# Performance work log

Measured on AMD Instinct MI355X. Metric: run time of the kernel, lower is better.

Reference implementation:

```python
import jax, jax.numpy as jnp
import numpy as np

D = 256  # feature_dim
NQ = 512
NK = 512


def setup_inputs() -> dict:
    key = jax.random.key(0)
    ks = jax.random.split(key, 12)
    s = 0.05
    return {
        "x": jax.random.normal(ks[0], (1, D, NQ), dtype=jnp.float32),
        "source": jax.random.normal(ks[1], (1, D, NK), dtype=jnp.float32),
        "dist": jax.random.normal(ks[2], (1, D, NQ * NK), dtype=jnp.float32),
        "mask": jax.random.randint(ks[3], (NQ, NK), 0, 2).astype(jnp.bool_),
        # MLPAttention mlp: channels [3D, D, 1] (1x1 convs == per-position matmuls)
        "aW1": jax.random.normal(ks[4], (D, 3 * D), dtype=jnp.float32) * s,
        "ab1": jax.random.normal(ks[5], (D,), dtype=jnp.float32) * s,
        "aW2": jax.random.normal(ks[6], (1, D), dtype=jnp.float32) * s,
        "ab2": jax.random.normal(ks[7], (1,), dtype=jnp.float32) * s,
        # merge mlp: channels [2D, 2D, D], last bias initialized to 0
        "mW1": jax.random.normal(ks[8], (2 * D, 2 * D), dtype=jnp.float32) * s,
        "mb1": jax.random.normal(ks[9], (2 * D,), dtype=jnp.float32) * s,
        "mW2": jax.random.normal(ks[10], (D, 2 * D), dtype=jnp.float32) * s,
        "mb2": jnp.zeros((D,), dtype=jnp.float32),
    }


def _conv1x1(W, b, x):
    # Conv1d(kernel_size=1): (out,in) @ (b,in,n) -> (b,out,n)
    return jnp.einsum('oc,bcn->bon', W, x) + b[None, :, None]


def reference(x, source, dist, mask, aW1, ab1, aW2, ab2, mW1, mb1, mW2, mb2):
    nq, nk = x.shape[-1], source.shape[-1]
    d = x.shape[1]
    # broadcast query over keys and key over queries, flatten to (1, d, nq*nk)
    qb = jnp.broadcast_to(x[:, :, :, None], (1, d, nq, nk)).reshape(1, d, nq * nk)
    kb = jnp.broadcast_to(source[:, :, None, :], (1, d, nq, nk)).reshape(1, d, nq * nk)
    feat = jnp.concatenate([qb, kb, dist], axis=1)  # (1, 3d, nq*nk)
    h = jax.nn.relu(_conv1x1(aW1, ab1, feat))       # (1, d, nq*nk)
    scores = _conv1x1(aW2, ab2, h).reshape(1, nq, nk)
    # boolean-mask branch: push masked-out entries far below the min
    neg = jax.lax.stop_gradient(scores.min()) - 20.0
    scores = scores + neg * (~mask).astype(scores.dtype)[None]
    prob = jax.nn.softmax(scores, axis=-1)
    message = jnp.einsum('bnm,bdm->bdn', prob, source)  # value == source
    # merge MLP on concat([x, message])
    cat = jnp.concatenate([x, message], axis=1)  # (1, 2d, nq)
    h2 = jax.nn.relu(_conv1x1(mW1, mb1, cat))
    out = _conv1x1(mW2, mb2, h2)  # (1, d, nq)
    return (out, scores)
```

## Files before the change

kernel.cpp:

```cpp
#include <hip/hip_runtime.h>
#include <stdint.h>

#define D_ 256
#define NQ_ 512
#define NK_ 512
#define NP_ (NQ_*NK_)

typedef __attribute__((ext_vector_type(8))) __bf16 bf16x8;
typedef __attribute__((ext_vector_type(4))) float f32x4;

__device__ __forceinline__ unsigned short f2bf(float f) {
  unsigned u = __builtin_bit_cast(unsigned, f);
  u += 0x7FFFu + ((u >> 16) & 1u);
  return (unsigned short)(u >> 16);
}
__device__ __forceinline__ unsigned encf(float f) {
  unsigned u = __builtin_bit_cast(unsigned, f);
  return (u & 0x80000000u) ? ~u : (u | 0x80000000u);
}
__device__ __forceinline__ float decf(unsigned e) {
  unsigned u = (e & 0x80000000u) ? (e ^ 0x80000000u) : ~e;
  return __builtin_bit_cast(float, u);
}

template<int EPI, int KTILES>
__device__ __forceinline__ void gemm_body(
    const unsigned short* __restrict__ A, int lda,
    const unsigned short* __restrict__ B, int ldb,
    const float* __restrict__ bias,
    void* __restrict__ Dst, int ldd, int nTilesN, int bid) {
  const int t = threadIdx.x, w = t >> 6, l = t & 63, l15 = l & 15, g = l >> 4;
  const int bm = bid / nTilesN, bn = bid % nTilesN;
  const int m0 = bm*64 + w*16, n0 = bn*64;
  const unsigned short* Ap = A + (size_t)(m0 + l15)*lda + g*8;
  const unsigned short* Bp = B + (size_t)(n0 + l15)*ldb + g*8;
  f32x4 acc[4];
  #pragma unroll
  for (int n = 0; n < 4; ++n) acc[n] = (f32x4){0.f,0.f,0.f,0.f};
  #pragma unroll 2
  for (int kk = 0; kk < KTILES; ++kk) {
    bf16x8 a = *(const bf16x8*)(Ap + kk*32);
    #pragma unroll
    for (int n = 0; n < 4; ++n) {
      bf16x8 b = *(const bf16x8*)(Bp + (size_t)n*16*ldb + kk*32);
      acc[n] = __builtin_amdgcn_mfma_f32_16x16x32_bf16(a, b, acc[n], 0, 0, 0);
    }
  }
  #pragma unroll
  for (int n = 0; n < 4; ++n) {
    const int col = n0 + n*16 + l15;
    const float bc = (EPI & 4) ? bias[col] : 0.f;
    #pragma unroll
    for (int r = 0; r < 4; ++r) {
      const int m = m0 + g*4 + r;
      float v = acc[n][r] + bc;
      if (EPI & 8) v += bias[m];
      if (EPI & 2) v = fmaxf(v, 0.f);
      if (EPI & 1) ((unsigned short*)Dst)[(size_t)m*ldd + col] = f2bf(v);
      else         ((float*)Dst)[(size_t)m*ldd + col] = v;
    }
  }
}

template<int EPI, int KTILES>
__global__ __launch_bounds__(256) void gemm_k(
    const unsigned short* __restrict__ A, int lda,
    const unsigned short* __restrict__ B, int ldb,
    const float* __restrict__ bias,
    void* __restrict__ Dst, int ldd, int nTilesN) {
  gemm_body<EPI, KTILES>(A, lda, B, ldb, bias, Dst, ldd, nTilesN, blockIdx.x);
}

__global__ __launch_bounds__(256) void kprep(
    const unsigned* __restrict__ maskw, unsigned* __restrict__ wsMin,
    unsigned* __restrict__ wsFlag,
    const float* __restrict__ aW1, const float* __restrict__ source,
    const float* __restrict__ x, const float* __restrict__ mW1,
    const float* __restrict__ mW2,
    unsigned short* __restrict__ Cb, unsigned short* __restrict__ srcbf,
    unsigned short* __restrict__ mW1b, unsigned short* __restrict__ mW2b,
    unsigned short* __restrict__ aW1A, unsigned short* __restrict__ aW1B,
    unsigned short* __restrict__ catT, unsigned short* __restrict__ srcT) {
  __shared__ float tile[64][65];
  const int b = blockIdx.x, t = threadIdx.x;
  if (b == 0) {
    if (t < 64) {
      unsigned a01 = 1, af = 1;
      for (int i = 0; i < 4; ++i) {
        unsigned v = maskw[t*4 + i];
        a01 &= (v == 0u || v == 1u) ? 1u : 0u;
        af  &= (v == 0u || v == 0x3f800000u) ? 1u : 0u;
      }
      unsigned long long b01 = __ballot(a01 != 0), bf = __ballot(af != 0);
      if (t == 0) {
        *wsFlag = (b01 == ~0ull) ? 1u : ((bf == ~0ull) ? 2u : 0u);
        *wsMin = 0xFFFFFFFFu;
      }
    }
    return;
  }
  if (b < 705) {
    const int bb = b - 1;
    const float* src; unsigned short* dst;
    if (bb < 64)        { int j = bb*1024 + t*4;       int e=j>>8, c=j&255; src = aW1 + e*768 + 512 + c; dst = Cb + j; }
    else if (bb < 192)  { int j = (bb-64)*1024 + t*4;  src = source + j;    dst = srcbf + j; }
    else if (bb < 448)  { int j = (bb-192)*1024 + t*4; src = mW1 + j;       dst = mW1b + j; }
    else if (bb < 576)  { int j = (bb-448)*1024 + t*4; src = mW2 + j;       dst = mW2b + j; }
    else if (bb < 640)  { int j = (bb-576)*1024 + t*4; int e=j>>8, c=j&255; src = aW1 + e*768 + c;       dst = aW1A + j; }
    else                { int j = (bb-640)*1024 + t*4; int e=j>>8, c=j&255; src = aW1 + e*768 + 256 + c; dst = aW1B + j; }
    const float4 v = *(const float4*)src;
    ushort4 o; o.x=f2bf(v.x); o.y=f2bf(v.y); o.z=f2bf(v.z); o.w=f2bf(v.w);
    *(ushort4*)dst = o;
    return;
  }
  const float* src; unsigned short* dst; int ldd, bid;
  if (b < 737) { src = x;      dst = catT; ldd = 512; bid = b - 705; }
  else         { src = source; dst = srcT; ldd = 256; bid = b - 737; }
  const int bd = bid >> 3, bq = bid & 7;
  const int r = t >> 4, c4 = (t & 15) * 4;
  #pragma unroll
  for (int rr = 0; rr < 4; ++rr) {
    int dl = rr*16 + r;
    float4 v = *(const float4*)(src + (size_t)(bd*64 + dl)*512 + bq*64 + c4);
    tile[dl][c4+0] = v.x; tile[dl][c4+1] = v.y; tile[dl][c4+2] = v.z; tile[dl][c4+3] = v.w;
  }
  __syncthreads();
  #pragma unroll
  for (int rr = 0; rr < 4; ++rr) {
    int j = rr*16 + r;
    ushort4 o;
    o.x = f2bf(tile[c4+0][j]); o.y = f2bf(tile[c4+1][j]);
    o.z = f2bf(tile[c4+2][j]); o.w = f2bf(tile[c4+3][j]);
    *(ushort4*)(dst + (size_t)(bq*64 + j)*ldd + bd*64 + c4) = o;
  }
}

__global__ __launch_bounds__(256) void kprep2(
    const unsigned short* __restrict__ catT, const unsigned short* __restrict__ aW1A,
    const float* __restrict__ ab1, float* __restrict__ Up,
    const unsigned short* __restrict__ aW1B, const unsigned short* __restrict__ srcT,
    float* __restrict__ Vm) {
  if (blockIdx.x < 32)
    gemm_body<4, 8>(catT, 512, aW1A, 256, ab1, (void*)Up, 256, 4, blockIdx.x);
  else
    gemm_body<0, 8>(aW1B, 256, srcT, 256, (const float*)nullptr, (void*)Vm, 512, 8, blockIdx.x - 32);
}

__device__ __forceinline__ void loads8(float (&s)[8], const float* __restrict__ dbase,
                                       int kk, int quad1, int quad2) {
  #pragma unroll
  for (int i = 0; i < 4; ++i) s[i]   = dbase[(size_t)(kk*32 + quad1*4 + i) * NP_];
  #pragma unroll
  for (int i = 0; i < 4; ++i) s[4+i] = dbase[(size_t)(kk*32 + quad2*4 + i) * NP_];
}
__device__ __forceinline__ void cvtwrite(unsigned char* __restrict__ buf, const float (&s)[8],
                                         int l, int quad1, int quad2) {
  const int key = (l >> 1) & 3;
  {
    unsigned lo = (unsigned)f2bf(s[0]) | ((unsigned)f2bf(s[1]) << 16);
    unsigned hi = (unsigned)f2bf(s[2]) | ((unsigned)f2bf(s[3]) << 16);
    *(uint2*)(buf + l*64 + ((((quad1>>1) ^ key) << 4) | ((quad1 & 1) << 3))) = make_uint2(lo, hi);
  }
  {
    unsigned lo = (unsigned)f2bf(s[4]) | ((unsigned)f2bf(s[5]) << 16);
    unsigned hi = (unsigned)f2bf(s[6]) | ((unsigned)f2bf(s[7]) << 16);
    *(uint2*)(buf + l*64 + ((((quad2>>1) ^ key) << 4) | ((quad2 & 1) << 3))) = make_uint2(lo, hi);
  }
}
__device__ __forceinline__ void computeStep(f32x4 (&acc)[4][4],
                                            const unsigned short* __restrict__ Abase,
                                            const unsigned char* __restrict__ buf,
                                            int kk, int l15, int g) {
  bf16x8 a[4], bfrag[4];
  #pragma unroll
  for (int m = 0; m < 4; ++m)
    a[m] = *(const bf16x8*)(Abase + (size_t)m*16*256 + kk*32);
  #pragma unroll
  for (int n = 0; n < 4; ++n) {
    const int p = n*16 + l15;
    bfrag[n] = *(const bf16x8*)(buf + p*64 + ((g ^ ((p >> 1) & 3)) << 4));
  }
  #pragma unroll
  for (int m = 0; m < 4; ++m)
    #pragma unroll
    for (int n = 0; n < 4; ++n)
      acc[m][n] = __builtin_amdgcn_mfma_f32_16x16x32_bf16(a[m], bfrag[n], acc[m][n], 0, 0, 0);
}

__global__ __launch_bounds__(256, 3) void kscores(
    const float* __restrict__ dist, const unsigned short* __restrict__ Cb,
    const float* __restrict__ Up, const float* __restrict__ Vm,
    const float* __restrict__ aW2, const float* __restrict__ ab2,
    float* __restrict__ outScores, unsigned* __restrict__ wsMin) {
  __shared__ __align__(16) unsigned char ldsB[2][64*64];
  __shared__ float u_s[256], aw2_s[256];
  __shared__ float red[4][64];

  const int t = threadIdx.x;
  const int w = t >> 6;
  const int l = t & 63;
  const int l15 = l & 15;
  const int g = l >> 4;

  const int bid = blockIdx.x;
  const int p0 = ((bid & 7) * 512 + (bid >> 3)) * 64;
  const int q  = p0 >> 9;
  const int k0 = p0 & 511;

  const int quad1 = (w + g) & 3;
  const int quad2 = quad1 + 4;

  const float* dbase = dist + (size_t)p0 + l;
  const unsigned short* Abase = Cb + (size_t)(w*64 + l15)*256 + g*8;

  float sA[8], sB[8];
  loads8(sA, dbase, 0, quad1, quad2);
  loads8(sB, dbase, 1, quad1, quad2);

  u_s[t]   = Up[q*256 + t];
  aw2_s[t] = aW2[t];

  f32x4 acc[4][4];
  #pragma unroll
  for (int m = 0; m < 4; ++m)
    #pragma unroll
    for (int n = 0; n < 4; ++n) acc[m][n] = (f32x4){0.f, 0.f, 0.f, 0.f};

  cvtwrite(ldsB[0], sA, l, quad1, quad2);
  __syncthreads();

  #pragma unroll
  for (int kk = 0; kk < 8; ++kk) {
    const int b = kk & 1;
    if (kk < 6) {
      if (b == 0) loads8(sA, dbase, kk + 2, quad1, quad2);
      else        loads8(sB, dbase, kk + 2, quad1, quad2);
    }
    computeStep(acc, Abase, ldsB[b], kk, l15, g);
    if (kk < 7) {
      if (b == 0) cvtwrite(ldsB[1], sB, l, quad1, quad2);
      else        cvtwrite(ldsB[0], sA, l, quad1, quad2);
    }
    __syncthreads();
  }

  float part[4];
  #pragma unroll
  for (int n = 0; n < 4; ++n) {
    int j = k0 + n*16 + l15;
    float s = 0.f;
    #pragma unroll
    for (int m = 0; m < 4; ++m) {
      #pragma unroll
      for (int r = 0; r < 4; ++r) {
        int e = w*64 + m*16 + g*4 + r;
        float gv = acc[m][n][r] + u_s[e] + Vm[e*512 + j];
        s += aw2_s[e] * fmaxf(gv, 0.f);
      }
    }
    s += __shfl_xor(s, 16);
    s += __shfl_xor(s, 32);
    part[n] = s;
  }
  if (l < 16) {
    #pragma unroll
    for (int n = 0; n < 4; ++n) red[w][n*16 + l] = part[n];
  }
  __syncthreads();
  if (t < 64) {
    float s = red[0][t] + red[1][t] + red[2][t] + red[3][t] + ab2[0];
    outScores[p0 + t] = s;
    float mn = s;
    #pragma unroll
    for (int off = 32; off; off >>= 1) mn = fminf(mn, __shfl_xor(mn, off));
    if (t == 0) atomicMin(wsMin, encf(mn));
  }
}

__global__ __launch_bounds__(256) void ksoftmax(
    const void* __restrict__ maskp,
    const unsigned* __restrict__ wsMin, const unsigned* __restrict__ wsFlag,
    float* __restrict__ scores, unsigned short* __restrict__ prob) {
  __shared__ float srow[512];
  __shared__ float redl[8];
  const int t = threadIdx.x, w = t >> 6, l = t & 63;
  const int q = blockIdx.x;
  const float neg = decf(*wsMin) - 20.0f;
  const unsigned flag = *wsFlag;

  for (int k = t; k < 512; k += 256) {
    float raw = scores[q*512 + k];
    bool mv;
    if (flag == 1)      mv = ((const int*)maskp)[q*512 + k] != 0;
    else if (flag == 2) mv = ((const float*)maskp)[q*512 + k] != 0.f;
    else                mv = ((const unsigned char*)maskp)[q*512 + k] != 0;
    float ms = raw + (mv ? 0.f : neg);
    scores[q*512 + k] = ms;
    srow[k] = ms;
  }
  __syncthreads();
  float lm = fmaxf(srow[t], srow[t + 256]);
  #pragma unroll
  for (int off = 32; off; off >>= 1) lm = fmaxf(lm, __shfl_xor(lm, off));
  if (l == 0) redl[w] = lm;
  __syncthreads();
  float rmax = fmaxf(fmaxf(redl[0], redl[1]), fmaxf(redl[2], redl[3]));
  float e0 = __expf(srow[t] - rmax), e1 = __expf(srow[t + 256] - rmax);
  float ls = e0 + e1;
  #pragma unroll
  for (int off = 32; off; off >>= 1) ls += __shfl_xor(ls, off);
  if (l == 0) redl[4 + w] = ls;
  __syncthreads();
  float inv = 1.0f / (redl[4] + redl[5] + redl[6] + redl[7]);
  prob[q*512 + t]       = f2bf(e0 * inv);
  prob[q*512 + t + 256] = f2bf(e1 * inv);
}

extern "C" void kernel_launch(void* const* d_in, const int* in_sizes, int n_in,
                              void* d_out, int out_size, void* d_ws, size_t ws_size,
                              hipStream_t stream) {
  const float* x      = (const float*)d_in[0];
  const float* source = (const float*)d_in[1];
  const float* dist   = (const float*)d_in[2];
  const void*  mask   = (const void*)d_in[3];
  const float* aW1    = (const float*)d_in[4];
  const float* ab1    = (const float*)d_in[5];
  const float* aW2    = (const float*)d_in[6];
  const float* ab2    = (const float*)d_in[7];
  const float* mW1    = (const float*)d_in[8];
  const float* mb1    = (const float*)d_in[9];
  const float* mW2    = (const float*)d_in[10];
  const float* mb2    = (const float*)d_in[11];

  float* outMain = (float*)d_out;
  float* scores  = outMain + 256*512;

  char* ws = (char*)d_ws;
  unsigned* wsMin  = (unsigned*)ws;
  unsigned* wsFlag = wsMin + 1;
  unsigned short* Cb    = (unsigned short*)(ws + 1024);
  float*          Up    = (float*)(ws + 132096);
  float*          Vm    = (float*)(ws + 656384);
  unsigned short* srcbf = (unsigned short*)(ws + 1180672);
  unsigned short* srcT  = (unsigned short*)(ws + 1442816);
  unsigned short* mW1b  = (unsigned short*)(ws + 1704960);
  unsigned short* mW2b  = (unsigned short*)(ws + 2229248);
  unsigned short* aW1A  = (unsigned short*)(ws + 2491392);
  unsigned short* aW1B  = (unsigned short*)(ws + 2622464);
  unsigned short* catT  = (unsigned short*)(ws + 2753536);
  unsigned short* prob  = (unsigned short*)(ws + 3277824);
  unsigned short* h2T   = (unsigned short*)(ws + 3802112);

  hipLaunchKernelGGL(kprep, dim3(769), dim3(256), 0, stream,
                     (const unsigned*)mask, wsMin, wsFlag, aW1, source, x, mW1, mW2,
                     Cb, srcbf, mW1b, mW2b, aW1A, aW1B, catT, srcT);
  hipLaunchKernelGGL(kprep2, dim3(64), dim3(256), 0, stream,
                     catT, aW1A, ab1, Up, aW1B, srcT, Vm);
  hipLaunchKernelGGL(kscores, dim3(4096), dim3(256), 0, stream,
                     dist, Cb, Up, Vm, aW2, ab2, scores, wsMin);
  hipLaunchKernelGGL(ksoftmax, dim3(512), dim3(256), 0, stream,
                     mask, wsMin, wsFlag, scores, prob);
  hipLaunchKernelGGL((gemm_k<1, 16>), dim3(32), dim3(256), 0, stream,
                     prob, 512, srcbf, 512, (const float*)nullptr, (void*)(catT + 256), 512, 4);
  hipLaunchKernelGGL((gemm_k<7, 16>), dim3(64), dim3(256), 0, stream,
                     catT, 512, mW1b, 512, mb1, (void*)h2T, 512, 8);
  hipLaunchKernelGGL((gemm_k<8, 16>), dim3(32), dim3(256), 0, stream,
                     mW2b, 512, h2T, 512, mb2, (void*)outMain, 512, 8);
}
```

Measured before the change: 186.5 us.

## Deepen dist prefetch to three stages and double-buffer A fragments

Restructures the kscores main loop to keep three register buffers of dist loads in flight instead of two, and prefetches the next step's A (weight) fragments into registers while the current step's MFMAs run. Explicit sched_barriers, an lgkmcnt wait and a raw s_barrier replace the trailing __syncthreads so the LDS write, next global loads and compute are ordered manually. This aims to hide global-load latency of the dist stream, at the cost of more VGPRs, which may reduce occupancy under launch_bounds(256,3). Because only one barrier now separates the LDS write of a buffer from later reads, reusing that buffer two steps later may be racy.

```diff
diff --git a/kernel.cpp b/kernel.cpp
--- a/kernel.cpp
+++ b/kernel.cpp
@@ -167,14 +167,16 @@
     *(uint2*)(buf + l*64 + ((((quad2>>1) ^ key) << 4) | ((quad2 & 1) << 3))) = make_uint2(lo, hi);
   }
 }
-__device__ __forceinline__ void computeStep(f32x4 (&acc)[4][4],
-                                            const unsigned short* __restrict__ Abase,
-                                            const unsigned char* __restrict__ buf,
-                                            int kk, int l15, int g) {
-  bf16x8 a[4], bfrag[4];
+__device__ __forceinline__ void loadA(bf16x8 (&a)[4], const unsigned short* __restrict__ Abase,
+                                      int kk) {
   #pragma unroll
   for (int m = 0; m < 4; ++m)
     a[m] = *(const bf16x8*)(Abase + (size_t)m*16*256 + kk*32);
+}
+__device__ __forceinline__ void computeStep(f32x4 (&acc)[4][4], const bf16x8 (&a)[4],
+                                            const unsigned char* __restrict__ buf,
+                                            int l15, int g) {
+  bf16x8 bfrag[4];
   #pragma unroll
   for (int n = 0; n < 4; ++n) {
     const int p = n*16 + l15;
@@ -213,54 +215,55 @@
   const float* dbase = dist + (size_t)p0 + l;
   const unsigned short* Abase = Cb + (size_t)(w*64 + l15)*256 + g*8;
 
-  float sA[8], sB[8];
-  loads8(sA, dbase, 0, quad1, quad2);
-  loads8(sB, dbase, 1, quad1, quad2);
-
-  u_s[t]   = Up[q*256 + t];
-  aw2_s[t] = aW2[t];
+  const float upv = Up[q*256 + t];
+  const float awv = aW2[t];
+  u_s[t]   = upv;
+  aw2_s[t] = awv;
+  __builtin_amdgcn_sched_barrier(0);
+
+  float s[3][8];
+  loads8(s[0], dbase, 0, quad1, quad2);
+  loads8(s[1], dbase, 1, quad1, quad2);
+  loads8(s[2], dbase, 2, quad1, quad2);
+  bf16x8 af[2][4];
+  loadA(af[0], Abase, 0);
 
   f32x4 acc[4][4];
   #pragma unroll
   for (int m = 0; m < 4; ++m)
     #pragma unroll
     for (int n = 0; n < 4; ++n) acc[m][n] = (f32x4){0.f, 0.f, 0.f, 0.f};
-
-  cvtwrite(ldsB[0], sA, l, quad1, quad2);
-  __syncthreads();
 
   #pragma unroll
   for (int kk = 0; kk < 8; ++kk) {
     const int b = kk & 1;
-    if (kk < 6) {
-      if (b == 0) loads8(sA, dbase, kk + 2, quad1, quad2);
-      else        loads8(sB, dbase, kk + 2, quad1, quad2);
-    }
-    computeStep(acc, Abase, ldsB[b], kk, l15, g);
-    if (kk < 7) {
-      if (b == 0) cvtwrite(ldsB[1], sB, l, quad1, quad2);
-      else        cvtwrite(ldsB[0], sA, l, quad1, quad2);
-    }
-    __syncthreads();
+    cvtwrite(ldsB[b], s[kk % 3], l, quad1, quad2);
+    if (kk < 5) loads8(s[kk % 3], dbase, kk + 3, quad1, quad2);
+    __builtin_amdgcn_sched_barrier(0);
+    asm volatile("s_waitcnt lgkmcnt(0)" ::: "memory");
+    __builtin_amdgcn_s_barrier();
+    __builtin_amdgcn_sched_barrier(0);
+    if (kk < 7) loadA(af[(kk + 1) & 1], Abase, kk + 1);
+    computeStep(acc, af[b], ldsB[b], l15, g);
   }
 
   float part[4];
   #pragma unroll
   for (int n = 0; n < 4; ++n) {
     int j = k0 + n*16 + l15;
-    float s = 0.f;
+    float s2 = 0.f;
     #pragma unroll
     for (int m = 0; m < 4; ++m) {
       #pragma unroll
       for (int r = 0; r < 4; ++r) {
         int e = w*64 + m*16 + g*4 + r;
         float gv = acc[m][n][r] + u_s[e] + Vm[e*512 + j];
-        s += aw2_s[e] * fmaxf(gv, 0.f);
+        s2 += aw2_s[e] * fmaxf(gv, 0.f);
       }
     }
-    s += __shfl_xor(s, 16);
-    s += __shfl_xor(s, 32);
-    part[n] = s;
+    s2 += __shfl_xor(s2, 16);
+    s2 += __shfl_xor(s2, 32);
+    part[n] = s2;
   }
   if (l < 16) {
     #pragma unroll
@@ -268,9 +271,9 @@
   }
   __syncthreads();
   if (t < 64) {
-    float s = red[0][t] + red[1][t] + red[2][t] + red[3][t] + ab2[0];
-    outScores[p0 + t] = s;
-    float mn = s;
+    float s2 = red[0][t] + red[1][t] + red[2][t] + red[3][t] + ab2[0];
+    outScores[p0 + t] = s2;
+    float mn = s2;
     #pragma unroll
     for (int off = 32; off; off >>= 1) mn = fminf(mn, __shfl_xor(mn, off));
     if (t == 0) atomicMin(wsMin, encf(mn));
```

Measured after the change: 206.3 us. 1.11x slower.
